# Optimization experiments

Measured on AMD Instinct MI355X. Metric: run time of the kernel, lower is better.

## Reference

```python
import jax, jax.numpy as jnp
import numpy as np

M_CHK, N_VAR, DV = 576, 1152, 3  # (3,x)-regular-column LDPC, rate 1/2
PI = 3.1415926


def _build_bp_matrices():
    """Vectorized replica of GetMatrixForBPNet (same math, no Python O(E^2) loops)."""
    rng = np.random.default_rng(0)
    H = np.zeros((M_CHK, N_VAR), np.float32)
    rows = np.argsort(rng.random((N_VAR, M_CHK)), axis=1)[:, :DV]  # DV distinct rows per column
    H[rows.ravel(), np.repeat(np.arange(N_VAR), DV)] = 1.0
    ii, jj = np.nonzero(H)                 # row-major edge list (sorted by row, then col)
    E = ii.size
    p_r2l = np.lexsort((ii, jj))           # Map_row_to_line: col-major position -> row-major index
    p_l2r = np.argsort(p_r2l)              # Map_line_to_row: inverse permutation
    cols_cm = jj[p_r2l]                    # column of each edge in col-major ("line") order
    # variable-node sum excluding self, in col-major order, then permute row-major input -> col-major
    S_V = (cols_cm[:, None] == cols_cm[None, :]).astype(np.float32)
    np.fill_diagonal(S_V, 0.0)
    H_sumV_to_C = np.zeros((E, E), np.float32)
    H_sumV_to_C[:, p_r2l] = S_V
    # check-node sum excluding self, in row-major order, then permute col-major input -> row-major
    S_C = (ii[:, None] == ii[None, :]).astype(np.float32)
    np.fill_diagonal(S_C, 0.0)
    H_sumC_to_V = np.zeros((E, E), np.float32)
    H_sumC_to_V[:, p_l2r] = S_C
    # llr -> per-edge init (col-major order)
    H_x_to_xe0 = np.zeros((E, N_VAR), np.float32)
    H_x_to_xe0[np.arange(E), cols_cm] = 1.0
    # per-variable sum of final edge messages (row-major input -> col-major sum)
    A = (np.arange(N_VAR)[:, None] == cols_cm[None, :]).astype(np.float32)
    H_xe_v_sumc_to_y = np.zeros((N_VAR, E), np.float32)
    H_xe_v_sumc_to_y[:, p_r2l] = A
    return H_x_to_xe0, H_sumC_to_V, H_sumV_to_C, H_xe_v_sumc_to_y


def setup_inputs() -> dict:
    key = jax.random.key(0)
    H_x_to_xe0, H_sumC_to_V, H_sumV_to_C, H_xe_v_sumc_to_y = _build_bp_matrices()
    llr_in = 2.0 * jax.random.normal(key, (16, N_VAR), dtype=jnp.float32)
    return {
        "llr_in": llr_in,
        "H_x_to_xe0": jnp.asarray(H_x_to_xe0),
        "H_sumC_to_V": jnp.asarray(H_sumC_to_V),
        "H_sumV_to_C": jnp.asarray(H_sumV_to_C),
        "H_xe_v_sumc_to_y": jnp.asarray(H_xe_v_sumc_to_y),
        "bp_iter_num": 8,
    }


def _one_bp_iteration(xe_v2c, xe_0, H_sumC_to_V, H_sumV_to_C):
    xe_tanh = jnp.tanh(xe_v2c / 2.0)
    sgn = jnp.sign(xe_tanh)
    # log-domain product over check-node neighbors (excluding self) via complex log trick
    sum_log_img = H_sumC_to_V @ ((1.0 - sgn) * (0.5 * PI))
    sum_log_real = H_sumC_to_V @ jnp.log(1e-8 + jnp.abs(xe_tanh))
    xe_product = jnp.exp(sum_log_real) * jnp.cos(sum_log_img)  # Re(exp(r + i*theta))
    xe_pd = xe_product + jnp.sign(xe_product) * (-2e-7)
    # 2 * atanh(x) with the module's custom atanh = 0.5*log((1+x)/(1-x+1e-10))
    xe_v_sumc = jnp.log((1.0 + xe_pd) / (1.0 - xe_pd + 1e-10))
    xe_c_sumv = xe_0 + H_sumV_to_C @ xe_v_sumc
    return xe_v_sumc, xe_c_sumv


def reference(llr_in, H_x_to_xe0, H_sumC_to_V, H_sumV_to_C, H_xe_v_sumc_to_y, bp_iter_num):
    llr_t = llr_in.T                      # [n, batch]
    xe_0 = H_x_to_xe0 @ llr_t             # [E, batch]
    xe_v2c = xe_0
    for _ in range(bp_iter_num - 1):
        _, xe_v2c = _one_bp_iteration(xe_v2c, xe_0, H_sumC_to_V, H_sumV_to_C)
    xe_v_sumc, _ = _one_bp_iteration(xe_v2c, xe_0, H_sumC_to_V, H_sumV_to_C)
    bp_out_llr = llr_t + H_xe_v_sumc_to_y @ xe_v_sumc
    dec_out = (1 - jnp.sign(bp_out_llr).astype(jnp.int32)) // 2
    return dec_out.T
```

## Files before the change

### kernel.cpp

```cpp
#include <hip/hip_runtime.h>

#define NV 1152
#define MC 576
#define NE 3456
#define MAXD 24
#define F4PART 3328
#define NF4IT 13

__global__ void k_p(const float* __restrict__ Hy, int* __restrict__ p_r2l) {
    const int wave = threadIdx.x >> 6, lane = threadIdx.x & 63;
    const int v = blockIdx.x * 4 + wave;
    if (v >= NV) return;
    const float* row = Hy + (size_t)v * NE;
    const float4* row4 = (const float4*)row;
    const unsigned long long below = (1ull << lane) - 1ull;
    int running = 0;
    for (int it = 0; it < NF4IT; ++it) {
        float4 val = row4[it * 64 + lane];
        unsigned long long m0 = __ballot(val.x != 0.0f);
        unsigned long long m1 = __ballot(val.y != 0.0f);
        unsigned long long m2 = __ballot(val.z != 0.0f);
        unsigned long long m3 = __ballot(val.w != 0.0f);
        int cb = __popcll(m0 & below) + __popcll(m1 & below)
               + __popcll(m2 & below) + __popcll(m3 & below);
        int base = it * 256 + 4 * lane;
        int b0 = (int)((m0 >> lane) & 1), b1 = (int)((m1 >> lane) & 1), b2 = (int)((m2 >> lane) & 1);
        if (val.x != 0.0f) { int p = running + cb;            if (p < 3) p_r2l[3 * v + p] = base; }
        if (val.y != 0.0f) { int p = running + cb + b0;       if (p < 3) p_r2l[3 * v + p] = base + 1; }
        if (val.z != 0.0f) { int p = running + cb + b0 + b1;  if (p < 3) p_r2l[3 * v + p] = base + 2; }
        if (val.w != 0.0f) { int p = running + cb + b0 + b1 + b2; if (p < 3) p_r2l[3 * v + p] = base + 3; }
        running += __popcll(m0) + __popcll(m1) + __popcll(m2) + __popcll(m3);
    }
    for (int base = F4PART; base < NE; base += 64) {
        float v0 = row[base + lane];
        unsigned long long m = __ballot(v0 != 0.0f);
        if (v0 != 0.0f) { int p = running + __popcll(m & below); if (p < 3) p_r2l[3 * v + p] = base + lane; }
        running += __popcll(m);
    }
}

__global__ void k_neigh(const float* __restrict__ Hc, const int* __restrict__ p_r2l,
                        int* __restrict__ neigh, int* __restrict__ deg) {
    const int wave = threadIdx.x >> 6, lane = threadIdx.x & 63;
    const int e = blockIdx.x * 4 + wave;
    if (e >= NE) return;
    const float* row = Hc + (size_t)p_r2l[e] * NE;
    const float4* row4 = (const float4*)row;
    const unsigned long long below = (1ull << lane) - 1ull;
    int running = 0;
    int* nl = neigh + (size_t)e * MAXD;
    for (int it = 0; it < NF4IT; ++it) {
        float4 val = row4[it * 64 + lane];
        unsigned long long m0 = __ballot(val.x != 0.0f);
        unsigned long long m1 = __ballot(val.y != 0.0f);
        unsigned long long m2 = __ballot(val.z != 0.0f);
        unsigned long long m3 = __ballot(val.w != 0.0f);
        int cb = __popcll(m0 & below) + __popcll(m1 & below)
               + __popcll(m2 & below) + __popcll(m3 & below);
        int base = it * 256 + 4 * lane;
        int b0 = (int)((m0 >> lane) & 1), b1 = (int)((m1 >> lane) & 1), b2 = (int)((m2 >> lane) & 1);
        if (val.x != 0.0f) { int p = running + cb;                if (p < MAXD) nl[p] = base; }
        if (val.y != 0.0f) { int p = running + cb + b0;           if (p < MAXD) nl[p] = base + 1; }
        if (val.z != 0.0f) { int p = running + cb + b0 + b1;      if (p < MAXD) nl[p] = base + 2; }
        if (val.w != 0.0f) { int p = running + cb + b0 + b1 + b2; if (p < MAXD) nl[p] = base + 3; }
        running += __popcll(m0) + __popcll(m1) + __popcll(m2) + __popcll(m3);
    }
    for (int base = F4PART; base < NE; base += 64) {
        float v0 = row[base + lane];
        unsigned long long m = __ballot(v0 != 0.0f);
        if (v0 != 0.0f) { int p = running + __popcll(m & below); if (p < MAXD) nl[p] = base + lane; }
        running += __popcll(m);
    }
    if (lane == 0) {
        int d = (running < MAXD) ? running : MAXD;
        int dp = (d + 7) & ~7;
        if (dp > MAXD) dp = MAXD;
        for (int j = d; j < dp; j++) nl[j] = NE;
        deg[e] = dp;
    }
}

__global__ __launch_bounds__(1024, 4) void k_bp(const float* __restrict__ llr_in,
                                                const int* __restrict__ neigh,
                                                const int* __restrict__ deg_g,
                                                const int* __restrict__ iter_ptr,
                                                int* __restrict__ out) {
    __shared__ float lr[NE + 1];
    __shared__ float li[NE + 1];
    __shared__ float msg[NE];
    __shared__ float llr_s[NV];
    const int b = blockIdx.x, t = threadIdx.x;
    const int iters = iter_ptr[0];
    for (int v = t; v < NV; v += 1024) llr_s[v] = llr_in[b * NV + v];
    if (t == 0) { lr[NE] = 0.0f; li[NE] = 0.0f; }
    __syncthreads();
    const int nk = (t < NE - 3 * 1024) ? 4 : 3;
    float xv[4], xb[4];
    int dgp[4], o1i[4], o2i[4];
    #pragma unroll
    for (int k = 0; k < 4; k++) {
        if (k < nk) {
            int e = t + k * 1024, v = e / 3, r = e - 3 * v;
            xb[k] = llr_s[v];
            xv[k] = xb[k];
            dgp[k] = deg_g[e];
            o1i[k] = 3 * v + ((r == 0) ? 1 : 0);
            o2i[k] = 3 * v + ((r == 2) ? 1 : 2);
        }
    }
    for (int it = 0; it < iters; ++it) {
        #pragma unroll
        for (int k = 0; k < 4; k++) {
            if (k < nk) {
                int e = t + k * 1024;
                float tv = tanhf(0.5f * xv[k]);
                float sgn = (tv > 0.0f) ? 1.0f : ((tv < 0.0f) ? -1.0f : 0.0f);
                lr[e] = logf(1e-8f + fabsf(tv));
                li[e] = (1.0f - sgn) * 1.5707963f;
            }
        }
        __syncthreads();
        #pragma unroll
        for (int k = 0; k < 4; k++) {
            if (k < nk) {
                int e = t + k * 1024;
                float slr = 0.0f, sli = 0.0f;
                const int* nl = neigh + (size_t)e * MAXD;
                const int dp = dgp[k];
                for (int j = 0; j < dp; j += 8) {
                    int i0 = nl[j], i1 = nl[j + 1], i2 = nl[j + 2], i3 = nl[j + 3];
                    int i4 = nl[j + 4], i5 = nl[j + 5], i6 = nl[j + 6], i7 = nl[j + 7];
                    slr += lr[i0]; sli += li[i0];
                    slr += lr[i1]; sli += li[i1];
                    slr += lr[i2]; sli += li[i2];
                    slr += lr[i3]; sli += li[i3];
                    slr += lr[i4]; sli += li[i4];
                    slr += lr[i5]; sli += li[i5];
                    slr += lr[i6]; sli += li[i6];
                    slr += lr[i7]; sli += li[i7];
                }
                float p = expf(slr) * cosf(sli);
                float ps = (p > 0.0f) ? 1.0f : ((p < 0.0f) ? -1.0f : 0.0f);
                float pd = p - 2e-7f * ps;
                msg[e] = logf((1.0f + pd) / ((1.0f - pd) + 1e-10f));
            }
        }
        __syncthreads();
        if (it + 1 < iters) {
            #pragma unroll
            for (int k = 0; k < 4; k++)
                if (k < nk) xv[k] = xb[k] + (msg[o1i[k]] + msg[o2i[k]]);
        }
    }
    for (int v = t; v < NV; v += 1024) {
        float S = (msg[3 * v] + msg[3 * v + 1]) + msg[3 * v + 2];
        out[b * NV + v] = ((llr_s[v] + S) < 0.0f) ? 1 : 0;
    }
}

extern "C" void kernel_launch(void* const* d_in, const int* in_sizes, int n_in,
                              void* d_out, int out_size, void* d_ws, size_t ws_size,
                              hipStream_t stream) {
    const float* llr_in = (const float*)d_in[0];
    const float* Hc2v   = (const float*)d_in[2];
    const float* Hy     = (const float*)d_in[4];
    const int*   iters  = (const int*)d_in[5];
    const int batch = in_sizes[0] / NV;
    int* p_r2l = (int*)d_ws;
    int* deg   = p_r2l + NE;
    int* neigh = deg + NE;
    hipLaunchKernelGGL(k_p, dim3((NV + 3) / 4), dim3(256), 0, stream, Hy, p_r2l);
    hipLaunchKernelGGL(k_neigh, dim3((NE + 3) / 4), dim3(256), 0, stream, Hc2v, p_r2l, neigh, deg);
    hipLaunchKernelGGL(k_bp, dim3(batch), dim3(1024), 0, stream,
                       llr_in, neigh, deg, iters, (int*)d_out);
}
```

Measured before the change: 197.9 us.

## Derive check-node adjacency from permutation instead of scanning full E×E matrix

Replaces the per-edge scan of the dense 3456×3456 check-to-variable matrix with one flat scan of the smaller variable-sum matrix using atomics. A single-block kernel then reconstructs the row/column permutations and check-row segments through sparse probes and a prefix scan. This avoids reading roughly 48 MB of dense matrix. The BP kernel also switches to 16-bit neighbour indices loaded as uint4 and interleaved float2 log/angle shared arrays, cutting index traffic and LDS load count. Risks: the atomic slot order is nondeterministic, so each column's entries are sorted explicitly, and the single-block build kernel is serial.

```diff
diff --git a/kernel.cpp b/kernel.cpp
--- a/kernel.cpp
+++ b/kernel.cpp
@@ -4,106 +4,115 @@
 #define MC 576
 #define NE 3456
 #define MAXD 24
-#define F4PART 3328
-#define NF4IT 13
+#define NF4 995328
 
-__global__ void k_p(const float* __restrict__ Hy, int* __restrict__ p_r2l) {
-    const int wave = threadIdx.x >> 6, lane = threadIdx.x & 63;
-    const int v = blockIdx.x * 4 + wave;
-    if (v >= NV) return;
-    const float* row = Hy + (size_t)v * NE;
-    const float4* row4 = (const float4*)row;
-    const unsigned long long below = (1ull << lane) - 1ull;
-    int running = 0;
-    for (int it = 0; it < NF4IT; ++it) {
-        float4 val = row4[it * 64 + lane];
-        unsigned long long m0 = __ballot(val.x != 0.0f);
-        unsigned long long m1 = __ballot(val.y != 0.0f);
-        unsigned long long m2 = __ballot(val.z != 0.0f);
-        unsigned long long m3 = __ballot(val.w != 0.0f);
-        int cb = __popcll(m0 & below) + __popcll(m1 & below)
-               + __popcll(m2 & below) + __popcll(m3 & below);
-        int base = it * 256 + 4 * lane;
-        int b0 = (int)((m0 >> lane) & 1), b1 = (int)((m1 >> lane) & 1), b2 = (int)((m2 >> lane) & 1);
-        if (val.x != 0.0f) { int p = running + cb;            if (p < 3) p_r2l[3 * v + p] = base; }
-        if (val.y != 0.0f) { int p = running + cb + b0;       if (p < 3) p_r2l[3 * v + p] = base + 1; }
-        if (val.z != 0.0f) { int p = running + cb + b0 + b1;  if (p < 3) p_r2l[3 * v + p] = base + 2; }
-        if (val.w != 0.0f) { int p = running + cb + b0 + b1 + b2; if (p < 3) p_r2l[3 * v + p] = base + 3; }
-        running += __popcll(m0) + __popcll(m1) + __popcll(m2) + __popcll(m3);
-    }
-    for (int base = F4PART; base < NE; base += 64) {
-        float v0 = row[base + lane];
-        unsigned long long m = __ballot(v0 != 0.0f);
-        if (v0 != 0.0f) { int p = running + __popcll(m & below); if (p < 3) p_r2l[3 * v + p] = base + lane; }
-        running += __popcll(m);
-    }
+__global__ void k_scan(const float* __restrict__ Hy, int* __restrict__ cnt,
+                       int* __restrict__ tri) {
+    int gid = blockIdx.x * 256 + threadIdx.x;
+    if (gid >= NF4) return;
+    float4 q = ((const float4*)Hy)[gid];
+    int f = 4 * gid;
+    if (q.x != 0.0f) { int v = f / NE;       int s = atomicAdd(&cnt[v], 1); if (s < 3) tri[3 * v + s] = f - v * NE; }
+    if (q.y != 0.0f) { int v = (f + 1) / NE; int s = atomicAdd(&cnt[v], 1); if (s < 3) tri[3 * v + s] = (f + 1) - v * NE; }
+    if (q.z != 0.0f) { int v = (f + 2) / NE; int s = atomicAdd(&cnt[v], 1); if (s < 3) tri[3 * v + s] = (f + 2) - v * NE; }
+    if (q.w != 0.0f) { int v = (f + 3) / NE; int s = atomicAdd(&cnt[v], 1); if (s < 3) tri[3 * v + s] = (f + 3) - v * NE; }
 }
 
-__global__ void k_neigh(const float* __restrict__ Hc, const int* __restrict__ p_r2l,
-                        int* __restrict__ neigh, int* __restrict__ deg) {
-    const int wave = threadIdx.x >> 6, lane = threadIdx.x & 63;
-    const int e = blockIdx.x * 4 + wave;
-    if (e >= NE) return;
-    const float* row = Hc + (size_t)p_r2l[e] * NE;
-    const float4* row4 = (const float4*)row;
-    const unsigned long long below = (1ull << lane) - 1ull;
-    int running = 0;
-    int* nl = neigh + (size_t)e * MAXD;
-    for (int it = 0; it < NF4IT; ++it) {
-        float4 val = row4[it * 64 + lane];
-        unsigned long long m0 = __ballot(val.x != 0.0f);
-        unsigned long long m1 = __ballot(val.y != 0.0f);
-        unsigned long long m2 = __ballot(val.z != 0.0f);
-        unsigned long long m3 = __ballot(val.w != 0.0f);
-        int cb = __popcll(m0 & below) + __popcll(m1 & below)
-               + __popcll(m2 & below) + __popcll(m3 & below);
-        int base = it * 256 + 4 * lane;
-        int b0 = (int)((m0 >> lane) & 1), b1 = (int)((m1 >> lane) & 1), b2 = (int)((m2 >> lane) & 1);
-        if (val.x != 0.0f) { int p = running + cb;                if (p < MAXD) nl[p] = base; }
-        if (val.y != 0.0f) { int p = running + cb + b0;           if (p < MAXD) nl[p] = base + 1; }
-        if (val.z != 0.0f) { int p = running + cb + b0 + b1;      if (p < MAXD) nl[p] = base + 2; }
-        if (val.w != 0.0f) { int p = running + cb + b0 + b1 + b2; if (p < MAXD) nl[p] = base + 3; }
-        running += __popcll(m0) + __popcll(m1) + __popcll(m2) + __popcll(m3);
+__global__ __launch_bounds__(1024) void k_build(const float* __restrict__ Hc,
+                                                const int* __restrict__ tri,
+                                                unsigned short* __restrict__ neigh,
+                                                int* __restrict__ deg) {
+    __shared__ int p_r2l[NE];
+    __shared__ unsigned short p_l2r[NE];
+    __shared__ unsigned short rowid[NE];
+    __shared__ unsigned short flag[NE];
+    __shared__ int rs[MC + 1];
+    __shared__ int partial[1024];
+    const int t = threadIdx.x;
+    for (int v = t; v < NV; v += 1024) {
+        int a = tri[3 * v], b = tri[3 * v + 1], c = tri[3 * v + 2];
+        int lo = min(a, min(b, c));
+        int hi = max(a, max(b, c));
+        int mid = a + b + c - lo - hi;
+        p_r2l[3 * v] = lo;  p_r2l[3 * v + 1] = mid;  p_r2l[3 * v + 2] = hi;
+        p_l2r[lo] = (unsigned short)(3 * v);
+        p_l2r[mid] = (unsigned short)(3 * v + 1);
+        p_l2r[hi] = (unsigned short)(3 * v + 2);
     }
-    for (int base = F4PART; base < NE; base += 64) {
-        float v0 = row[base + lane];
-        unsigned long long m = __ballot(v0 != 0.0f);
-        if (v0 != 0.0f) { int p = running + __popcll(m & below); if (p < MAXD) nl[p] = base + lane; }
-        running += __popcll(m);
+    __syncthreads();
+    for (int a = t; a < NE; a += 1024) {
+        int fl = 0;
+        if (a > 0) fl = (Hc[(size_t)(a - 1) * NE + (int)p_l2r[a]] == 0.0f) ? 1 : 0;
+        flag[a] = (unsigned short)fl;
     }
-    if (lane == 0) {
-        int d = (running < MAXD) ? running : MAXD;
-        int dp = (d + 7) & ~7;
+    __syncthreads();
+    int inc[4];
+    int run = 0;
+    const int base4 = t * 4;
+    #pragma unroll
+    for (int k = 0; k < 4; k++) {
+        int idx = base4 + k;
+        run += (idx < NE) ? (int)flag[idx] : 0;
+        inc[k] = run;
+    }
+    partial[t] = run;
+    __syncthreads();
+    for (int off = 1; off < 1024; off <<= 1) {
+        int add = (t >= off) ? partial[t - off] : 0;
+        __syncthreads();
+        partial[t] += add;
+        __syncthreads();
+    }
+    int prev = (t > 0) ? partial[t - 1] : 0;
+    #pragma unroll
+    for (int k = 0; k < 4; k++) {
+        int idx = base4 + k;
+        if (idx < NE) rowid[idx] = (unsigned short)(prev + inc[k]);
+    }
+    __syncthreads();
+    for (int a = t; a < NE; a += 1024)
+        if (a == 0 || flag[a]) rs[rowid[a]] = a;
+    if (t == 0) rs[(int)rowid[NE - 1] + 1] = NE;
+    __syncthreads();
+    for (int e = t; e < NE; e += 1024) {
+        int a = p_r2l[e];
+        int r = rowid[a];
+        int s = rs[r], en = rs[r + 1];
+        unsigned short* nl = neigh + (size_t)e * MAXD;
+        int pos = 0;
+        for (int a2 = s; a2 < en; ++a2) {
+            if (a2 != a && pos < MAXD) nl[pos++] = p_l2r[a2];
+        }
+        int dp = (pos + 7) & ~7;
         if (dp > MAXD) dp = MAXD;
-        for (int j = d; j < dp; j++) nl[j] = NE;
+        for (int j = pos; j < dp; j++) nl[j] = NE;
         deg[e] = dp;
     }
 }
 
 __global__ __launch_bounds__(1024, 4) void k_bp(const float* __restrict__ llr_in,
-                                                const int* __restrict__ neigh,
+                                                const unsigned short* __restrict__ neigh,
                                                 const int* __restrict__ deg_g,
                                                 const int* __restrict__ iter_ptr,
                                                 int* __restrict__ out) {
-    __shared__ float lr[NE + 1];
-    __shared__ float li[NE + 1];
+    __shared__ float2 lrli[NE + 1];
     __shared__ float msg[NE];
     __shared__ float llr_s[NV];
     const int b = blockIdx.x, t = threadIdx.x;
     const int iters = iter_ptr[0];
     for (int v = t; v < NV; v += 1024) llr_s[v] = llr_in[b * NV + v];
-    if (t == 0) { lr[NE] = 0.0f; li[NE] = 0.0f; }
+    if (t == 0) lrli[NE] = make_float2(0.0f, 0.0f);
     __syncthreads();
     const int nk = (t < NE - 3 * 1024) ? 4 : 3;
     float xv[4], xb[4];
-    int dgp[4], o1i[4], o2i[4];
+    int nch[4], o1i[4], o2i[4];
     #pragma unroll
     for (int k = 0; k < 4; k++) {
         if (k < nk) {
             int e = t + k * 1024, v = e / 3, r = e - 3 * v;
             xb[k] = llr_s[v];
             xv[k] = xb[k];
-            dgp[k] = deg_g[e];
+            nch[k] = deg_g[e] >> 3;
             o1i[k] = 3 * v + ((r == 0) ? 1 : 0);
             o2i[k] = 3 * v + ((r == 2) ? 1 : 2);
         }
@@ -115,8 +124,8 @@
                 int e = t + k * 1024;
                 float tv = tanhf(0.5f * xv[k]);
                 float sgn = (tv > 0.0f) ? 1.0f : ((tv < 0.0f) ? -1.0f : 0.0f);
-                lr[e] = logf(1e-8f + fabsf(tv));
-                li[e] = (1.0f - sgn) * 1.5707963f;
+                lrli[e] = make_float2(logf(1e-8f + fabsf(tv)),
+                                      (1.0f - sgn) * 1.5707963f);
             }
         }
         __syncthreads();
@@ -125,19 +134,24 @@
             if (k < nk) {
                 int e = t + k * 1024;
                 float slr = 0.0f, sli = 0.0f;
-                const int* nl = neigh + (size_t)e * MAXD;
-                const int dp = dgp[k];
-                for (int j = 0; j < dp; j += 8) {
-                    int i0 = nl[j], i1 = nl[j + 1], i2 = nl[j + 2], i3 = nl[j + 3];
-                    int i4 = nl[j + 4], i5 = nl[j + 5], i6 = nl[j + 6], i7 = nl[j + 7];
-                    slr += lr[i0]; sli += li[i0];
-                    slr += lr[i1]; sli += li[i1];
-                    slr += lr[i2]; sli += li[i2];
-                    slr += lr[i3]; sli += li[i3];
-                    slr += lr[i4]; sli += li[i4];
-                    slr += lr[i5]; sli += li[i5];
-                    slr += lr[i6]; sli += li[i6];
-                    slr += lr[i7]; sli += li[i7];
+                const uint4* nlp = (const uint4*)(neigh + (size_t)e * MAXD);
+                const int nc = nch[k];
+                for (int c = 0; c < nc; ++c) {
+                    uint4 q = nlp[c];
+                    int i0 = q.x & 0xFFFF, i1 = q.x >> 16;
+                    int i2 = q.y & 0xFFFF, i3 = q.y >> 16;
+                    int i4 = q.z & 0xFFFF, i5 = q.z >> 16;
+                    int i6 = q.w & 0xFFFF, i7 = q.w >> 16;
+                    float2 a0 = lrli[i0], a1 = lrli[i1], a2 = lrli[i2], a3 = lrli[i3];
+                    float2 a4 = lrli[i4], a5 = lrli[i5], a6 = lrli[i6], a7 = lrli[i7];
+                    slr += a0.x; sli += a0.y;
+                    slr += a1.x; sli += a1.y;
+                    slr += a2.x; sli += a2.y;
+                    slr += a3.x; sli += a3.y;
+                    slr += a4.x; sli += a4.y;
+                    slr += a5.x; sli += a5.y;
+                    slr += a6.x; sli += a6.y;
+                    slr += a7.x; sli += a7.y;
                 }
                 float p = expf(slr) * cosf(sli);
                 float ps = (p > 0.0f) ? 1.0f : ((p < 0.0f) ? -1.0f : 0.0f);
@@ -166,11 +180,14 @@
     const float* Hy     = (const float*)d_in[4];
     const int*   iters  = (const int*)d_in[5];
     const int batch = in_sizes[0] / NV;
-    int* p_r2l = (int*)d_ws;
-    int* deg   = p_r2l + NE;
-    int* neigh = deg + NE;
-    hipLaunchKernelGGL(k_p, dim3((NV + 3) / 4), dim3(256), 0, stream, Hy, p_r2l);
-    hipLaunchKernelGGL(k_neigh, dim3((NE + 3) / 4), dim3(256), 0, stream, Hc2v, p_r2l, neigh, deg);
+    char* ws = (char*)d_ws;
+    unsigned short* neigh = (unsigned short*)ws;
+    int* deg = (int*)(ws + NE * MAXD * sizeof(unsigned short));
+    int* cnt = deg + NE;
+    int* tri = cnt + NV;
+    hipMemsetAsync(cnt, 0, NV * sizeof(int), stream);
+    hipLaunchKernelGGL(k_scan, dim3((NF4 + 255) / 256), dim3(256), 0, stream, Hy, cnt, tri);
+    hipLaunchKernelGGL(k_build, dim3(1), dim3(1024), 0, stream, Hc2v, tri, neigh, deg);
     hipLaunchKernelGGL(k_bp, dim3(batch), dim3(1024), 0, stream,
                        llr_in, neigh, deg, iters, (int*)d_out);
 }
```

New measurement: 195.8 us. About the same (-1.0%).
